# Kernel optimization log

Measured on AMD Instinct MI355X. Metric: run time of the kernel, lower is better.

## Reference

```python
import jax, jax.numpy as jnp
import numpy as np

B, S, D_MODEL, D_Q = 16, 2048, 384, 64


def setup_inputs() -> dict:
    key = jax.random.key(0)
    k1, k2, k3, k4 = jax.random.split(key, 4)
    x = jax.random.normal(k1, (B, S, D_MODEL), dtype=jnp.float32)
    # nn.Linear(d_model, d_q, bias=False) weights, stored as [d_model, d_q] so q = x @ Wq
    scale = 1.0 / np.sqrt(D_MODEL)
    Wq = jax.random.normal(k2, (D_MODEL, D_Q), dtype=jnp.float32) * scale
    Wk = jax.random.normal(k3, (D_MODEL, D_Q), dtype=jnp.float32) * scale
    Wv = jax.random.normal(k4, (D_MODEL, D_Q), dtype=jnp.float32) * scale
    return {"x": x, "Wq": Wq, "Wk": Wk, "Wv": Wv}


def reference(x, Wq, Wk, Wv):
    # x: [B, S, d_model]
    q = jnp.einsum("bsd,de->bse", x, Wq)  # [B, S, d_q]
    k = jnp.einsum("bsd,de->bse", x, Wk)
    v = jnp.einsum("bsd,de->bse", x, Wv)
    d_q = q.shape[-1]
    # full S x S score matrix, scaled by sqrt(d_q) as in the torch code (k.size(-1)**0.5)
    scores = jnp.einsum("bse,bte->bst", q, k) / jnp.sqrt(jnp.float32(d_q))
    s = x.shape[1]
    causal = jnp.tril(jnp.ones((s, s), dtype=bool))  # [S, S]
    scores = jnp.where(causal, scores, jnp.float32(-jnp.inf))
    probs = jax.nn.softmax(scores, axis=-1)
    # dropout is identity in eval/reference mode
    out = jnp.einsum("bst,bte->bse", probs, v)  # [B, S, d_q]
    return out
```

## Files before the change

### kernel.cpp

```cpp
#include <hip/hip_runtime.h>
#include <hip/hip_bf16.h>
#include <math.h>

#define BB 16
#define SS 2048
#define DM 384
#define DQ 64
#define M_ROWS (BB * SS)

typedef short short8 __attribute__((ext_vector_type(8)));
typedef float f32x4  __attribute__((ext_vector_type(4)));

#define WT_OFF 0
#define QB_OFF 73728
#define KB_OFF (QB_OFF + M_ROWS * DQ)
#define VT_OFF (KB_OFF + M_ROWS * DQ)

#define QSCALE 0.18033688011112042f

__device__ __forceinline__ short f2bf(float f) {
  unsigned u = __builtin_bit_cast(unsigned, f);
  unsigned r = (u + 0x7fffu + ((u >> 16) & 1u)) >> 16;
  return (short)r;
}
__device__ __forceinline__ unsigned pack2bf(float a, float b) {
  return (unsigned)(unsigned short)f2bf(a) |
         ((unsigned)(unsigned short)f2bf(b) << 16);
}
__device__ __forceinline__ void async16(const short* g, short* l) {
  __builtin_amdgcn_global_load_lds(
      (const __attribute__((address_space(1))) unsigned int*)g,
      (__attribute__((address_space(3))) unsigned int*)l, 16, 0, 0);
}

__global__ void prep_w_kernel(const float* __restrict__ Wq,
                              const float* __restrict__ Wk,
                              const float* __restrict__ Wv,
                              short* __restrict__ ws) {
  int o = blockIdx.x * 256 + threadIdx.x;
  int mat = o / (DM * DQ);
  int r = o % (DM * DQ);
  int k = r / DQ, n = r % DQ;
  const float* W = (mat == 0) ? Wq : (mat == 1) ? Wk : Wv;
  ws[WT_OFF + mat * (DM * DQ) + n * DM + k] = f2bf(W[k * DQ + n]);
}

__global__ __launch_bounds__(256) void qkv_proj_mfma(
    const float* __restrict__ x, const short* __restrict__ ws_r,
    short* __restrict__ ws_w) {
  __shared__ short Wtc[2][12288];
  __shared__ short Ep[64 * 200];
  const int tid = threadIdx.x;
  const int lane = tid & 63, w = tid >> 6;
  const int cidx = lane & 15, g = lane >> 4;
  const int g8 = g * 8, g4 = g * 4;
  const int sw7 = cidx & 7;
  const int rows0 = blockIdx.x * 64;
  const short* Wt = ws_r + WT_OFF;

  const int prow = tid >> 3;
  const int pgr = tid & 7;
  const short* wsrc = Wt + (size_t)prow * DM + ((pgr ^ (prow & 7)) * 8);

  f32x4 acc[12];
  #pragma unroll
  for (int i = 0; i < 12; ++i) acc[i] = (f32x4){0.f, 0.f, 0.f, 0.f};

  const float* xr = x + (size_t)(rows0 + 16 * w + cidx) * DM;

  float4 xc0 = *(const float4*)(xr + g8);
  float4 xc1 = *(const float4*)(xr + g8 + 4);
  float4 xc2 = *(const float4*)(xr + 32 + g8);
  float4 xc3 = *(const float4*)(xr + 32 + g8 + 4);
  #pragma unroll
  for (int itr = 0; itr < 6; ++itr)
    async16(wsrc + (size_t)itr * 32 * DM, &Wtc[0][(itr * 256 + w * 64) * 8]);

  #pragma unroll
  for (int it = 0; it < 6; ++it) {
    __syncthreads();

    float4 xn0, xn1, xn2, xn3;
    if (it < 5) {
      const int k0n = (it + 1) * 64;
      #pragma unroll
      for (int itr = 0; itr < 6; ++itr)
        async16(wsrc + (size_t)itr * 32 * DM + k0n,
                &Wtc[(it + 1) & 1][(itr * 256 + w * 64) * 8]);
      xn0 = *(const float4*)(xr + k0n + g8);
      xn1 = *(const float4*)(xr + k0n + g8 + 4);
      xn2 = *(const float4*)(xr + k0n + 32 + g8);
      xn3 = *(const float4*)(xr + k0n + 32 + g8 + 4);
    }

    short8 a0, a1;
    a0[0]=f2bf(xc0.x); a0[1]=f2bf(xc0.y); a0[2]=f2bf(xc0.z); a0[3]=f2bf(xc0.w);
    a0[4]=f2bf(xc1.x); a0[5]=f2bf(xc1.y); a0[6]=f2bf(xc1.z); a0[7]=f2bf(xc1.w);
    a1[0]=f2bf(xc2.x); a1[1]=f2bf(xc2.y); a1[2]=f2bf(xc2.z); a1[3]=f2bf(xc2.w);
    a1[4]=f2bf(xc3.x); a1[5]=f2bf(xc3.y); a1[6]=f2bf(xc3.z); a1[7]=f2bf(xc3.w);

    const short* Wb = Wtc[it & 1];
    #pragma unroll
    for (int ct = 0; ct < 12; ++ct) {
      int row = ct * 16 + cidx;
      short8 b0 = *(const short8*)&Wb[row * 64 + ((g ^ sw7) * 8)];
      short8 b1 = *(const short8*)&Wb[row * 64 + (((g + 4) ^ sw7) * 8)];
      acc[ct] = __builtin_amdgcn_mfma_f32_16x16x32_bf16(a0, b0, acc[ct], 0, 0, 0);
      acc[ct] = __builtin_amdgcn_mfma_f32_16x16x32_bf16(a1, b1, acc[ct], 0, 0, 0);
    }
    if (it < 5) { xc0 = xn0; xc1 = xn1; xc2 = xn2; xc3 = xn3; }
  }

  __syncthreads();
  const int erow = 16 * w + g4;
  #pragma unroll
  for (int ct = 0; ct < 4; ++ct)
    #pragma unroll
    for (int r = 0; r < 4; ++r) {
      Ep[(erow + r) * 200 + ct * 16 + cidx]       = f2bf(acc[ct][r] * QSCALE);
      Ep[(erow + r) * 200 + 64 + ct * 16 + cidx]  = f2bf(acc[4 + ct][r]);
      Ep[(ct * 16 + cidx) * 200 + 128 + erow + r] = f2bf(acc[8 + ct][r]);
    }
  __syncthreads();

  short* Qb = ws_w + QB_OFF;
  short* Kb = ws_w + KB_OFF;
  short* Vt = ws_w + VT_OFF;
  const int bidx = rows0 >> 11;
  const int srow0 = rows0 & 2047;
  #pragma unroll
  for (int t2 = 0; t2 < 2; ++t2) {
    int i = t2 * 256 + tid;
    int row = i >> 3, gq = i & 7;
    *(short8*)&Qb[(size_t)(rows0 + row) * DQ + gq * 8] =
        *(const short8*)&Ep[row * 200 + gq * 8];
    *(short8*)&Kb[(size_t)(rows0 + row) * DQ + gq * 8] =
        *(const short8*)&Ep[row * 200 + 64 + gq * 8];
    *(short8*)&Vt[(size_t)bidx * (64 * SS) + (size_t)row * SS + srow0 + gq * 8] =
        *(const short8*)&Ep[row * 200 + 128 + gq * 8];
  }
}

__global__ __launch_bounds__(256, 4) void flash_mfma(
    const short* __restrict__ ws, float* __restrict__ O) {
  __shared__ short smem[18944];
  const int b = blockIdx.y;
  const int qt = (b < 8) ? (63 - (int)blockIdx.x) : (int)blockIdx.x;
  const int q0 = qt * 32;
  const int tid = threadIdx.x;
  const int lane = tid & 63, w = tid >> 6;
  const int qg = w & 1, s = w >> 1;
  const int cidx = lane & 15, g = lane >> 4;
  const int g8 = g * 8, g4 = g * 4;
  const int sw7 = cidx & 7;
  short* Ps = smem + 16384 + w * 640;

  const short* Qb = ws + QB_OFF + (size_t)b * SS * DQ;
  const short* Kb = ws + KB_OFF + (size_t)b * SS * DQ;
  const short* Vt = ws + VT_OFF + (size_t)b * 64 * SS;

  const int qrow = q0 + qg * 16;
  const int qglob = qrow + cidx;
  short8 qf0 = *(const short8*)&Qb[(size_t)qglob * DQ + g8];
  short8 qf1 = *(const short8*)&Qb[(size_t)qglob * DQ + 32 + g8];

  const int srow = tid >> 3;
  const int sgr = tid & 7;
  const int ssw = (sgr ^ (srow & 7)) * 8;
  const short* kb0 = Kb + (size_t)srow * DQ + ssw;
  const short* kb1 = Kb + (size_t)(srow + 32) * DQ + ssw;
  const short* vb0 = Vt + (size_t)srow * SS + ssw;
  const short* vb1 = Vt + (size_t)(srow + 32) * SS + ssw;
  const int dst0 = (w * 64) * 8, dst1 = (256 + w * 64) * 8;

  f32x4 o[4];
  #pragma unroll
  for (int i = 0; i < 4; ++i) o[i] = (f32x4){0.f, 0.f, 0.f, 0.f};
  float l = 0.f;

  const int nss = (qt >> 1) + 1;

  async16(kb0, &smem[dst0]);
  async16(kb1, &smem[dst1]);
  async16(vb0, &smem[8192 + dst0]);
  async16(vb1, &smem[8192 + dst1]);

  for (int ssi = 0; ssi < nss; ++ssi) {
    __syncthreads();

    {
      int nb = (ssi + 1) * 64;
      if (nb > SS - 64) nb = SS - 64;
      const int nbuf = ((ssi + 1) & 1) * 4096;
      const size_t koff = (size_t)nb * DQ;
      async16(kb0 + koff, &smem[nbuf + dst0]);
      async16(kb1 + koff, &smem[nbuf + dst1]);
      async16(vb0 + nb, &smem[8192 + nbuf + dst0]);
      async16(vb1 + nb, &smem[8192 + nbuf + dst1]);
    }

    const int kt32 = ssi * 2 + s;
    if (kt32 <= qt) {
      const short* Kc = smem + (ssi & 1) * 4096;
      const short* Vc = smem + 8192 + (ssi & 1) * 4096;
      const int kbase = ssi * 64;
      f32x4 sc[2];
      #pragma unroll
      for (int ct = 0; ct < 2; ++ct) {
        int krow = s * 32 + ct * 16 + cidx;
        short8 kf0 = *(const short8*)&Kc[krow * 64 + ((g ^ sw7) * 8)];
        short8 kf1 = *(const short8*)&Kc[krow * 64 + (((g + 4) ^ sw7) * 8)];
        f32x4 a = (f32x4){0.f, 0.f, 0.f, 0.f};
        a = __builtin_amdgcn_mfma_f32_16x16x32_bf16(kf0, qf0, a, 0, 0, 0);
        a = __builtin_amdgcn_mfma_f32_16x16x32_bf16(kf1, qf1, a, 0, 0, 0);
        sc[ct] = a;
      }
      if (kt32 == qt) {
        #pragma unroll
        for (int ct = 0; ct < 2; ++ct) {
          int key = kbase + s * 32 + ct * 16 + g4;
          #pragma unroll
          for (int r = 0; r < 4; ++r)
            if (key + r > qglob) sc[ct][r] = -1e30f;
        }
      }
      #pragma unroll
      for (int ct = 0; ct < 2; ++ct) {
        #pragma unroll
        for (int r = 0; r < 4; ++r) {
          float p = __builtin_amdgcn_exp2f(sc[ct][r]);
          sc[ct][r] = p;
          l += p;
        }
        uint2 pk;
        pk.x = pack2bf(sc[ct][0], sc[ct][1]);
        pk.y = pack2bf(sc[ct][2], sc[ct][3]);
        *(uint2*)&Ps[cidx * 40 + ct * 16 + g4] = pk;
      }
      short8 pf = *(const short8*)&Ps[cidx * 40 + g8];
      #pragma unroll
      for (int dt = 0; dt < 4; ++dt) {
        int vrow = dt * 16 + cidx;
        short8 vf = *(const short8*)&Vc[vrow * 64 + (((s * 4 + g) ^ sw7) * 8)];
        o[dt] = __builtin_amdgcn_mfma_f32_16x16x32_bf16(vf, pf, o[dt], 0, 0, 0);
      }
    }
  }

  l += __shfl_xor(l, 16);
  l += __shfl_xor(l, 32);

  float* o1x = (float*)smem;
  float* l1x = (float*)(smem + 4096);
  float* Of  = (float*)(smem + 4224);
  __syncthreads();
  if (s == 1) {
    int base = qg * 1024;
    #pragma unroll
    for (int dt = 0; dt < 4; ++dt)
      #pragma unroll
      for (int r = 0; r < 4; ++r)
        o1x[base + dt * 256 + r * 64 + lane] = o[dt][r];
    if (g == 0) l1x[qg * 16 + cidx] = l;
  }
  __syncthreads();
  if (s == 0) {
    int base = qg * 1024;
    float inv = 1.0f / (l + l1x[qg * 16 + cidx]);
    #pragma unroll
    for (int dt = 0; dt < 4; ++dt)
      #pragma unroll
      for (int r = 0; r < 4; ++r)
        Of[(qg * 16 + cidx) * 72 + dt * 16 + g4 + r] =
            (o[dt][r] + o1x[base + dt * 256 + r * 64 + lane]) * inv;
  }
  __syncthreads();
  #pragma unroll
  for (int t2 = 0; t2 < 2; ++t2) {
    int i = t2 * 256 + tid;
    int qb = i >> 4, f4 = i & 15;
    float4 v = *(const float4*)&Of[qb * 72 + f4 * 4];
    *(float4*)&O[((size_t)b * SS + q0 + qb) * DQ + f4 * 4] = v;
  }
}

extern "C" void kernel_launch(void* const* d_in, const int* in_sizes, int n_in,
                              void* d_out, int out_size, void* d_ws, size_t ws_size,
                              hipStream_t stream) {
  const float* x  = (const float*)d_in[0];
  const float* Wq = (const float*)d_in[1];
  const float* Wk = (const float*)d_in[2];
  const float* Wv = (const float*)d_in[3];
  short* ws = (short*)d_ws;
  float* out = (float*)d_out;

  prep_w_kernel<<<288, 256, 0, stream>>>(Wq, Wk, Wv, ws);
  qkv_proj_mfma<<<M_ROWS / 64, 256, 0, stream>>>(x, ws, ws);
  flash_mfma<<<dim3(64, BB), 256, 0, stream>>>(ws, out);
}
```

Before: 126.9 us.

## Use 64-row query tiles with one wave per 16 queries, drop split-K merge

The flash kernel now processes 64 queries per block, with each wave owning 16 query rows and the full 64-key tile. The old design split each key tile across two waves and merged partial outputs through shared memory, and that merge plus its extra barriers is removed. Outputs are written directly from registers. The projection kernel also drops its double-buffered W prefetch in favour of a simpler single-buffer load per k-step, which likely exposes more load latency. The flash grid halves to 512 blocks, which reduces parallelism and gives the diagonal blocks coarser masking.

Measured after the change: 126.6 us. About the same (-0.2%).

```diff
diff --git a/kernel.cpp b/kernel.cpp
--- a/kernel.cpp
+++ b/kernel.cpp
@@ -48,7 +48,7 @@
 __global__ __launch_bounds__(256) void qkv_proj_mfma(
     const float* __restrict__ x, const short* __restrict__ ws_r,
     short* __restrict__ ws_w) {
-  __shared__ short Wtc[2][12288];
+  __shared__ short Wtc[192 * 64];
   __shared__ short Ep[64 * 200];
   const int tid = threadIdx.x;
   const int lane = tid & 63, w = tid >> 6;
@@ -58,40 +58,26 @@
   const int rows0 = blockIdx.x * 64;
   const short* Wt = ws_r + WT_OFF;
 
-  const int prow = tid >> 3;
-  const int pgr = tid & 7;
-  const short* wsrc = Wt + (size_t)prow * DM + ((pgr ^ (prow & 7)) * 8);
-
   f32x4 acc[12];
   #pragma unroll
   for (int i = 0; i < 12; ++i) acc[i] = (f32x4){0.f, 0.f, 0.f, 0.f};
 
   const float* xr = x + (size_t)(rows0 + 16 * w + cidx) * DM;
 
-  float4 xc0 = *(const float4*)(xr + g8);
-  float4 xc1 = *(const float4*)(xr + g8 + 4);
-  float4 xc2 = *(const float4*)(xr + 32 + g8);
-  float4 xc3 = *(const float4*)(xr + 32 + g8 + 4);
-  #pragma unroll
-  for (int itr = 0; itr < 6; ++itr)
-    async16(wsrc + (size_t)itr * 32 * DM, &Wtc[0][(itr * 256 + w * 64) * 8]);
-
-  #pragma unroll
-  for (int it = 0; it < 6; ++it) {
+  for (int k0 = 0; k0 < DM; k0 += 64) {
+    float4 xc0 = *(const float4*)(xr + k0 + g8);
+    float4 xc1 = *(const float4*)(xr + k0 + g8 + 4);
+    float4 xc2 = *(const float4*)(xr + k0 + 32 + g8);
+    float4 xc3 = *(const float4*)(xr + k0 + 32 + g8 + 4);
     __syncthreads();
-
-    float4 xn0, xn1, xn2, xn3;
-    if (it < 5) {
-      const int k0n = (it + 1) * 64;
-      #pragma unroll
-      for (int itr = 0; itr < 6; ++itr)
-        async16(wsrc + (size_t)itr * 32 * DM + k0n,
-                &Wtc[(it + 1) & 1][(itr * 256 + w * 64) * 8]);
-      xn0 = *(const float4*)(xr + k0n + g8);
-      xn1 = *(const float4*)(xr + k0n + g8 + 4);
-      xn2 = *(const float4*)(xr + k0n + 32 + g8);
-      xn3 = *(const float4*)(xr + k0n + 32 + g8 + 4);
-    }
+    #pragma unroll
+    for (int it = 0; it < 6; ++it) {
+      int i = it * 256 + tid;
+      int row = i >> 3, gr = i & 7;
+      const short* src = Wt + row * DM + k0 + ((gr ^ (row & 7)) * 8);
+      async16(src, &Wtc[(it * 256 + w * 64) * 8]);
+    }
+    __syncthreads();
 
     short8 a0, a1;
     a0[0]=f2bf(xc0.x); a0[1]=f2bf(xc0.y); a0[2]=f2bf(xc0.z); a0[3]=f2bf(xc0.w);
@@ -99,16 +85,14 @@
     a1[0]=f2bf(xc2.x); a1[1]=f2bf(xc2.y); a1[2]=f2bf(xc2.z); a1[3]=f2bf(xc2.w);
     a1[4]=f2bf(xc3.x); a1[5]=f2bf(xc3.y); a1[6]=f2bf(xc3.z); a1[7]=f2bf(xc3.w);
 
-    const short* Wb = Wtc[it & 1];
     #pragma unroll
     for (int ct = 0; ct < 12; ++ct) {
       int row = ct * 16 + cidx;
-      short8 b0 = *(const short8*)&Wb[row * 64 + ((g ^ sw7) * 8)];
-      short8 b1 = *(const short8*)&Wb[row * 64 + (((g + 4) ^ sw7) * 8)];
+      short8 b0 = *(const short8*)&Wtc[row * 64 + ((g ^ sw7) * 8)];
+      short8 b1 = *(const short8*)&Wtc[row * 64 + (((g + 4) ^ sw7) * 8)];
       acc[ct] = __builtin_amdgcn_mfma_f32_16x16x32_bf16(a0, b0, acc[ct], 0, 0, 0);
       acc[ct] = __builtin_amdgcn_mfma_f32_16x16x32_bf16(a1, b1, acc[ct], 0, 0, 0);
     }
-    if (it < 5) { xc0 = xn0; xc1 = xn1; xc2 = xn2; xc3 = xn3; }
   }
 
   __syncthreads();
@@ -143,29 +127,28 @@
 
 __global__ __launch_bounds__(256, 4) void flash_mfma(
     const short* __restrict__ ws, float* __restrict__ O) {
-  __shared__ short smem[18944];
+  __shared__ short smem[20480];
   const int b = blockIdx.y;
-  const int qt = (b < 8) ? (63 - (int)blockIdx.x) : (int)blockIdx.x;
-  const int q0 = qt * 32;
+  const int qx = blockIdx.x;
+  const int qt = (b < 8) ? (31 - qx) : qx;
+  const int q0 = qt * 64;
   const int tid = threadIdx.x;
   const int lane = tid & 63, w = tid >> 6;
-  const int qg = w & 1, s = w >> 1;
   const int cidx = lane & 15, g = lane >> 4;
   const int g8 = g * 8, g4 = g * 4;
   const int sw7 = cidx & 7;
-  short* Ps = smem + 16384 + w * 640;
+  short* Ps = smem + 16384 + w * 1024;
 
   const short* Qb = ws + QB_OFF + (size_t)b * SS * DQ;
   const short* Kb = ws + KB_OFF + (size_t)b * SS * DQ;
   const short* Vt = ws + VT_OFF + (size_t)b * 64 * SS;
 
-  const int qrow = q0 + qg * 16;
+  const int qrow = q0 + w * 16;
   const int qglob = qrow + cidx;
   short8 qf0 = *(const short8*)&Qb[(size_t)qglob * DQ + g8];
   short8 qf1 = *(const short8*)&Qb[(size_t)qglob * DQ + 32 + g8];
 
-  const int srow = tid >> 3;
-  const int sgr = tid & 7;
+  const int srow = tid >> 3, sgr = tid & 7;
   const int ssw = (sgr ^ (srow & 7)) * 8;
   const short* kb0 = Kb + (size_t)srow * DQ + ssw;
   const short* kb1 = Kb + (size_t)(srow + 32) * DQ + ssw;
@@ -178,7 +161,7 @@
   for (int i = 0; i < 4; ++i) o[i] = (f32x4){0.f, 0.f, 0.f, 0.f};
   float l = 0.f;
 
-  const int nss = (qt >> 1) + 1;
+  const int nss = qt + 1;
 
   async16(kb0, &smem[dst0]);
   async16(kb1, &smem[dst1]);
@@ -190,7 +173,7 @@
 
     {
       int nb = (ssi + 1) * 64;
-      if (nb > SS - 64) nb = SS - 64;
+      if (nb > q0) nb = q0;
       const int nbuf = ((ssi + 1) & 1) * 4096;
       const size_t koff = (size_t)nb * DQ;
       async16(kb0 + koff, &smem[nbuf + dst0]);
@@ -199,49 +182,51 @@
       async16(vb1 + nb, &smem[8192 + nbuf + dst1]);
     }
 
-    const int kt32 = ssi * 2 + s;
-    if (kt32 <= qt) {
-      const short* Kc = smem + (ssi & 1) * 4096;
-      const short* Vc = smem + 8192 + (ssi & 1) * 4096;
-      const int kbase = ssi * 64;
-      f32x4 sc[2];
+    const short* Kc = smem + (ssi & 1) * 4096;
+    const short* Vc = smem + 8192 + (ssi & 1) * 4096;
+    const int kbase = ssi * 64;
+
+    f32x4 sc[4];
+    #pragma unroll
+    for (int ct = 0; ct < 4; ++ct) {
+      int krow = ct * 16 + cidx;
+      short8 kf0 = *(const short8*)&Kc[krow * 64 + ((g ^ sw7) * 8)];
+      short8 kf1 = *(const short8*)&Kc[krow * 64 + (((g + 4) ^ sw7) * 8)];
+      f32x4 a = (f32x4){0.f, 0.f, 0.f, 0.f};
+      a = __builtin_amdgcn_mfma_f32_16x16x32_bf16(kf0, qf0, a, 0, 0, 0);
+      a = __builtin_amdgcn_mfma_f32_16x16x32_bf16(kf1, qf1, a, 0, 0, 0);
+      sc[ct] = a;
+    }
+    if (ssi == nss - 1) {
       #pragma unroll
-      for (int ct = 0; ct < 2; ++ct) {
-        int krow = s * 32 + ct * 16 + cidx;
-        short8 kf0 = *(const short8*)&Kc[krow * 64 + ((g ^ sw7) * 8)];
-        short8 kf1 = *(const short8*)&Kc[krow * 64 + (((g + 4) ^ sw7) * 8)];
-        f32x4 a = (f32x4){0.f, 0.f, 0.f, 0.f};
-        a = __builtin_amdgcn_mfma_f32_16x16x32_bf16(kf0, qf0, a, 0, 0, 0);
-        a = __builtin_amdgcn_mfma_f32_16x16x32_bf16(kf1, qf1, a, 0, 0, 0);
-        sc[ct] = a;
+      for (int ct = 0; ct < 4; ++ct) {
+        int key = kbase + ct * 16 + g4;
+        #pragma unroll
+        for (int r = 0; r < 4; ++r)
+          if (key + r > qglob) sc[ct][r] = -1e30f;
       }
-      if (kt32 == qt) {
-        #pragma unroll
-        for (int ct = 0; ct < 2; ++ct) {
-          int key = kbase + s * 32 + ct * 16 + g4;
-          #pragma unroll
-          for (int r = 0; r < 4; ++r)
-            if (key + r > qglob) sc[ct][r] = -1e30f;
-        }
+    }
+    #pragma unroll
+    for (int ct = 0; ct < 4; ++ct) {
+      #pragma unroll
+      for (int r = 0; r < 4; ++r) {
+        float p = __builtin_amdgcn_exp2f(sc[ct][r]);
+        sc[ct][r] = p;
+        l += p;
       }
-      #pragma unroll
-      for (int ct = 0; ct < 2; ++ct) {
-        #pragma unroll
-        for (int r = 0; r < 4; ++r) {
-          float p = __builtin_amdgcn_exp2f(sc[ct][r]);
-          sc[ct][r] = p;
-          l += p;
-        }
-        uint2 pk;
-        pk.x = pack2bf(sc[ct][0], sc[ct][1]);
-        pk.y = pack2bf(sc[ct][2], sc[ct][3]);
-        *(uint2*)&Ps[cidx * 40 + ct * 16 + g4] = pk;
-      }
-      short8 pf = *(const short8*)&Ps[cidx * 40 + g8];
+      int gb = ct * 2 + (g >> 1);
+      uint2 pk;
+      pk.x = pack2bf(sc[ct][0], sc[ct][1]);
+      pk.y = pack2bf(sc[ct][2], sc[ct][3]);
+      *(uint2*)&Ps[cidx * 64 + ((gb ^ sw7) * 8) + (g & 1) * 4] = pk;
+    }
+    #pragma unroll
+    for (int ks = 0; ks < 2; ++ks) {
+      short8 pf = *(const short8*)&Ps[cidx * 64 + (((ks * 4 + g) ^ sw7) * 8)];
       #pragma unroll
       for (int dt = 0; dt < 4; ++dt) {
         int vrow = dt * 16 + cidx;
-        short8 vf = *(const short8*)&Vc[vrow * 64 + (((s * 4 + g) ^ sw7) * 8)];
+        short8 vf = *(const short8*)&Vc[vrow * 64 + (((ks * 4 + g) ^ sw7) * 8)];
         o[dt] = __builtin_amdgcn_mfma_f32_16x16x32_bf16(vf, pf, o[dt], 0, 0, 0);
       }
     }
@@ -249,38 +234,14 @@
 
   l += __shfl_xor(l, 16);
   l += __shfl_xor(l, 32);
-
-  float* o1x = (float*)smem;
-  float* l1x = (float*)(smem + 4096);
-  float* Of  = (float*)(smem + 4224);
-  __syncthreads();
-  if (s == 1) {
-    int base = qg * 1024;
-    #pragma unroll
-    for (int dt = 0; dt < 4; ++dt)
-      #pragma unroll
-      for (int r = 0; r < 4; ++r)
-        o1x[base + dt * 256 + r * 64 + lane] = o[dt][r];
-    if (g == 0) l1x[qg * 16 + cidx] = l;
-  }
-  __syncthreads();
-  if (s == 0) {
-    int base = qg * 1024;
-    float inv = 1.0f / (l + l1x[qg * 16 + cidx]);
-    #pragma unroll
-    for (int dt = 0; dt < 4; ++dt)
-      #pragma unroll
-      for (int r = 0; r < 4; ++r)
-        Of[(qg * 16 + cidx) * 72 + dt * 16 + g4 + r] =
-            (o[dt][r] + o1x[base + dt * 256 + r * 64 + lane]) * inv;
-  }
-  __syncthreads();
-  #pragma unroll
-  for (int t2 = 0; t2 < 2; ++t2) {
-    int i = t2 * 256 + tid;
-    int qb = i >> 4, f4 = i & 15;
-    float4 v = *(const float4*)&Of[qb * 72 + f4 * 4];
-    *(float4*)&O[((size_t)b * SS + q0 + qb) * DQ + f4 * 4] = v;
+  const float inv = 1.0f / l;
+
+  float* op = O + ((size_t)b * SS + qglob) * DQ;
+  #pragma unroll
+  for (int dt = 0; dt < 4; ++dt) {
+    float4 v = make_float4(o[dt][0] * inv, o[dt][1] * inv,
+                           o[dt][2] * inv, o[dt][3] * inv);
+    *(float4*)&op[dt * 16 + g4] = v;
   }
 }
 
@@ -296,5 +257,5 @@
 
   prep_w_kernel<<<288, 256, 0, stream>>>(Wq, Wk, Wv, ws);
   qkv_proj_mfma<<<M_ROWS / 64, 256, 0, stream>>>(x, ws, ws);
-  flash_mfma<<<dim3(64, BB), 256, 0, stream>>>(ws, out);
-}
+  flash_mfma<<<dim3(32, BB), 256, 0, stream>>>(ws, out);
+}
```
